# Performance work log

Hardware: AMD Instinct MI355X
Metric: run time of the kernel (lower is better)

Reference implementation:

```python
import jax, jax.numpy as jnp
import numpy as np

N, E, F, H = 50000, 500000, 128, 128   # nodes, edges, in-features, hidden
L, R, B = 3, 8, 30                     # layers, relations, bases
G, C = 16, 8                           # graphs in batch, classes
EPS = 1e-5


def setup_inputs() -> dict:
    key = jax.random.key(0)
    ks = jax.random.split(key, 16)
    x = jax.random.normal(ks[0], (N, F), jnp.float32)
    edge_index = jax.random.randint(ks[1], (2, E), 0, N)
    edge_attr = jax.random.randint(ks[2], (E,), 0, R)
    batch = jnp.sort(jax.random.randint(ks[3], (N,), 0, G))
    # RGCN params (all layers share shapes since F == H)
    basis = jax.random.normal(ks[4], (L, B, H, H), jnp.float32) * 0.05
    comp = jax.random.normal(ks[5], (L, R, B), jnp.float32) * 0.2
    root = jax.random.normal(ks[6], (L, H, H), jnp.float32) * 0.05
    bias = jnp.zeros((L, H), jnp.float32)
    # BatchNorm (eval mode: running stats)
    bn1_gamma = jnp.ones((F,), jnp.float32)
    bn1_beta = jnp.zeros((F,), jnp.float32)
    bn1_mean = jax.random.normal(ks[7], (F,), jnp.float32) * 0.1
    bn1_var = jax.random.uniform(ks[8], (F,), jnp.float32, 0.5, 1.5)
    bn2_gamma = jnp.ones((H,), jnp.float32)
    bn2_beta = jnp.zeros((H,), jnp.float32)
    bn2_mean = jax.random.normal(ks[9], (H,), jnp.float32) * 0.1
    bn2_var = jax.random.uniform(ks[10], (H,), jnp.float32, 0.5, 1.5)
    fc1_w = jax.random.normal(ks[11], (H, H), jnp.float32) * 0.05
    fc1_b = jnp.zeros((H,), jnp.float32)
    fc2_w = jax.random.normal(ks[12], (H, C), jnp.float32) * 0.05
    fc2_b = jnp.zeros((C,), jnp.float32)
    return dict(x=x, edge_index=edge_index, edge_attr=edge_attr, batch=batch,
                bn1_gamma=bn1_gamma, bn1_beta=bn1_beta, bn1_mean=bn1_mean, bn1_var=bn1_var,
                basis=basis, comp=comp, root=root, bias=bias,
                bn2_gamma=bn2_gamma, bn2_beta=bn2_beta, bn2_mean=bn2_mean, bn2_var=bn2_var,
                fc1_w=fc1_w, fc1_b=fc1_b, fc2_w=fc2_w, fc2_b=fc2_b)


def _bn(x, gamma, beta, mean, var):
    return (x - mean) * jax.lax.rsqrt(var + EPS) * gamma + beta


def _rgcn_layer(x, basis_l, comp_l, root_l, bias_l, src, dst, edge_attr):
    # root transform + bias
    out = x @ root_l + bias_l
    # relation-wise basis-decomposed message passing, mean-aggregated per relation
    for r in range(R):
        W_r = jnp.einsum('b,bio->io', comp_l[r], basis_l)  # [H, H]
        xw = x @ W_r                                       # [N, H]
        mask = (edge_attr == r).astype(x.dtype)            # [E]
        msg = xw[src] * mask[:, None]                      # gather + mask
        agg = jax.ops.segment_sum(msg, dst, num_segments=N)
        deg = jax.ops.segment_sum(mask, dst, num_segments=N)
        out = out + agg / jnp.maximum(deg, 1.0)[:, None]
    return out


def reference(x, edge_index, edge_attr, batch,
              bn1_gamma, bn1_beta, bn1_mean, bn1_var,
              basis, comp, root, bias,
              bn2_gamma, bn2_beta, bn2_mean, bn2_var,
              fc1_w, fc1_b, fc2_w, fc2_b):
    src, dst = edge_index[0], edge_index[1]
    h = _bn(x, bn1_gamma, bn1_beta, bn1_mean, bn1_var)
    for l in range(L):
        h = jax.nn.relu(_rgcn_layer(h, basis[l], comp[l], root[l], bias[l], src, dst, edge_attr))
        # dropout is identity in eval mode
    # global mean pool per graph
    sums = jax.ops.segment_sum(h, batch, num_segments=G)            # [G, H]
    counts = jax.ops.segment_sum(jnp.ones((N,), h.dtype), batch, num_segments=G)
    g = sums / jnp.maximum(counts, 1.0)[:, None]
    g = _bn(g, bn2_gamma, bn2_beta, bn2_mean, bn2_var)
    # temporal_type == 'mean'
    v = jax.nn.relu(g.mean(axis=0))                                 # [H]
    v = jax.nn.relu(v @ fc1_w + fc1_b)
    logits = v @ fc2_w + fc2_b                                      # [C]
    return jax.nn.log_softmax(logits, axis=-1)
```

## Files before the change

### kernel.cpp

```cpp
#include <hip/hip_runtime.h>
#include <hip/hip_bf16.h>

#define NN 50000
#define NE 500000
#define HID 128
#define LAYERS 3
#define RELS 8
#define BASES 30
#define GRAPHS 16
#define CLASSES 8
#define EPSV 1e-5f
#define NOUT (HID * (RELS + 1))
#define NSEG (NN * RELS)
#define SCAN_CHUNK 1024
#define SCAN_NBLK2 ((NSEG + SCAN_CHUNK - 1) / SCAN_CHUNK)
#define PCHUNK 128
#define DTILE 64
#define NDBLK ((NN + DTILE - 1) / DTILE)

typedef __attribute__((ext_vector_type(8))) short short8;
typedef __attribute__((ext_vector_type(4))) float f32x4;

__device__ __forceinline__ float bf2f(unsigned short u) {
    union { unsigned int i; float f; } x; x.i = ((unsigned int)u) << 16; return x.f;
}
__device__ __forceinline__ unsigned short f2bf(float f) {
    __hip_bfloat16 b = __float2bfloat16(f);
    return *(unsigned short*)&b;
}
__device__ __forceinline__ float ubf_lo(unsigned w) {
    union { unsigned i; float f; } t; t.i = w << 16; return t.f;
}
__device__ __forceinline__ float ubf_hi(unsigned w) {
    union { unsigned i; float f; } t; t.i = w & 0xFFFF0000u; return t.f;
}
__device__ __forceinline__ int permf(int f) {
    return (f & 64) | ((f & 15) << 2) | ((f >> 4) & 3);
}
__device__ __forceinline__ int ipermf(int q) {
    return (q & 64) | ((q & 3) << 4) | ((q >> 2) & 15);
}
__device__ __forceinline__ void gload16(const void* g, void* l) {
    __builtin_amdgcn_global_load_lds(
        (const __attribute__((address_space(1))) unsigned int*)g,
        (__attribute__((address_space(3))) unsigned int*)l, 16, 0, 0);
}

__global__ __launch_bounds__(256) void build_wcat(const float* __restrict__ basis,
                                                  const float* __restrict__ comp,
                                                  const float* __restrict__ root,
                                                  unsigned short* __restrict__ wT) {
    int bid = blockIdx.x;
    int l = bid >> 6;
    int k0 = (bid & 63) << 1;
    __shared__ float cl[RELS * BASES];
    int tid = threadIdx.x;
    if (tid < RELS * BASES) cl[tid] = comp[l * RELS * BASES + tid];
    __syncthreads();
    int j = tid & 127;
    int k = k0 + (tid >> 7);
    int pk = permf(k);
    const float* bp = basis + ((size_t)l * BASES * HID + k) * HID + j;
    float acc[RELS];
#pragma unroll
    for (int r = 0; r < RELS; ++r) acc[r] = 0.f;
    for (int b = 0; b < BASES; ++b) {
        float v = bp[(size_t)b * HID * HID];
#pragma unroll
        for (int r = 0; r < RELS; ++r) acc[r] += cl[r * BASES + b] * v;
    }
    unsigned short* wl = wT + (size_t)l * NOUT * HID;
#pragma unroll
    for (int r = 0; r < RELS; ++r)
        wl[(size_t)((1 + r) * HID + j) * HID + pk] = f2bf(acc[r]);
    wl[(size_t)j * HID + pk] = f2bf(root[((size_t)l * HID + k) * HID + j]);
}

__global__ void bn1_kernel(const float* __restrict__ x, const float* __restrict__ gamma,
                           const float* __restrict__ beta, const float* __restrict__ mean,
                           const float* __restrict__ var, unsigned short* __restrict__ habf) {
    int idx = blockIdx.x * blockDim.x + threadIdx.x;
    if (idx >= NN * HID) return;
    int q = idx & (HID - 1);
    int n = idx >> 7;
    int f = ipermf(q);
    habf[idx] = f2bf((x[(n << 7) + f] - mean[f]) * rsqrtf(var[f] + EPSV) * gamma[f] + beta[f]);
}

__global__ void deg_kernel(const int* __restrict__ ei, const int* __restrict__ ea,
                           float* __restrict__ deg) {
    int e = blockIdx.x * blockDim.x + threadIdx.x;
    if (e >= NE) return;
    int dst = ei[NE + e];
    atomicAdd(&deg[(size_t)dst * RELS + ea[e]], 1.0f);
}

__global__ __launch_bounds__(256) void scan_partial(float* __restrict__ deg,
                                                    int* __restrict__ rowptr,
                                                    int* __restrict__ bsum) {
    __shared__ int ssc[256];
    int t = threadIdx.x;
    int base = blockIdx.x * SCAN_CHUNK + t * 4;
    int v[4];
#pragma unroll
    for (int j = 0; j < 4; ++j) {
        int seg = base + j;
        if (seg < NSEG) {
            float d = deg[seg];
            v[j] = (int)(d + 0.5f);
            deg[seg] = 1.0f / fmaxf(d, 1.0f);
        } else v[j] = 0;
    }
    int tsum = v[0] + v[1] + v[2] + v[3];
    ssc[t] = tsum;
    __syncthreads();
    for (int ofs = 1; ofs < 256; ofs <<= 1) {
        int add = (t >= ofs) ? ssc[t - ofs] : 0;
        __syncthreads();
        ssc[t] += add;
        __syncthreads();
    }
    int excl = ssc[t] - tsum;
    int e = 0;
#pragma unroll
    for (int j = 0; j < 4; ++j) {
        if (base + j < NSEG) rowptr[base + j] = excl + e;
        e += v[j];
    }
    if (t == 255) bsum[blockIdx.x] = ssc[255];
}

__global__ __launch_bounds__(512) void scan_bsum(int* __restrict__ bsum) {
    __shared__ int s[512];
    int t = threadIdx.x;
    int v = (t < SCAN_NBLK2) ? bsum[t] : 0;
    s[t] = v;
    __syncthreads();
    for (int o = 1; o < 512; o <<= 1) {
        int a = (t >= o) ? s[t - o] : 0;
        __syncthreads();
        s[t] += a;
        __syncthreads();
    }
    if (t < SCAN_NBLK2) bsum[t] = s[t] - v;
}

__global__ __launch_bounds__(256) void scan_add(int* __restrict__ rowptr,
                                                const int* __restrict__ bsum) {
    int i = blockIdx.x * blockDim.x + threadIdx.x;
    if (i < NSEG) rowptr[i] += bsum[i >> 10];
    if (i == 0) rowptr[NSEG] = NE;
}

__global__ void fill_kernel(const int* __restrict__ ei, const int* __restrict__ ea,
                            const int* __restrict__ rowptr,
                            int* __restrict__ fillcnt, int* __restrict__ epk) {
    int e = blockIdx.x * blockDim.x + threadIdx.x;
    if (e >= NE) return;
    int src = ei[e];
    int seg = ei[NE + e] * RELS + ea[e];
    int pos = atomicAdd(&fillcnt[seg], 1);
    epk[rowptr[seg] + pos] = src;
}

__global__ __launch_bounds__(256) void rgcn_layer(const unsigned short* __restrict__ hin,
                                                  const unsigned short* __restrict__ wTl,
                                                  const float* __restrict__ bias,
                                                  const int* __restrict__ rp2,
                                                  const int* __restrict__ epk2,
                                                  const float* __restrict__ invdeg,
                                                  unsigned short* __restrict__ hout) {
    __shared__ __align__(16) unsigned short As[DTILE * HID];
    __shared__ __align__(16) unsigned short Bs[128 * HID];
    int row0 = blockIdx.x * DTILE;
    int tid = threadIdx.x;
    int wave = tid >> 6, lane = tid & 63;
    int quad = lane >> 4, l16 = lane & 15;
    int wn = wave * 32;
    int ld = tid >> 2, tq = tid & 3;
    int dst = row0 + ld;

    f32x4 acc[4][2];
#pragma unroll
    for (int i = 0; i < 4; ++i)
#pragma unroll
        for (int j = 0; j < 2; ++j) acc[i][j] = (f32x4){0.f, 0.f, 0.f, 0.f};

    auto mfma_panel = [&]() {
#pragma unroll
        for (int kc = 0; kc < 4; ++kc) {
            int ca = ((kc * 4 + quad) ^ (l16 & 7)) << 3;
            short8 a[4], b[2];
#pragma unroll
            for (int i = 0; i < 4; ++i) a[i] = *(const short8*)&As[(i * 16 + l16) * HID + ca];
#pragma unroll
            for (int j = 0; j < 2; ++j) b[j] = *(const short8*)&Bs[(wn + j * 16 + l16) * HID + ca];
#pragma unroll
            for (int i = 0; i < 4; ++i)
#pragma unroll
                for (int j = 0; j < 2; ++j)
                    acc[i][j] = __builtin_amdgcn_mfma_f32_16x16x32_bf16(a[i], b[j], acc[i][j], 0, 0, 0);
        }
    };

#pragma unroll
    for (int q = 0; q < 4; ++q) {
        int rb = (wave << 4) + (q << 2);
        int r = rb + (lane >> 4), c = lane & 15;
        int ga = row0 + r; if (ga > NN - 1) ga = NN - 1;
        gload16(hin + (size_t)ga * HID + ((c ^ (r & 7)) << 3), &As[rb * HID]);
    }
#pragma unroll
    for (int q = 0; q < 8; ++q) {
        int rb = (wave << 5) + (q << 2);
        int r = rb + (lane >> 4), c = lane & 15;
        gload16(wTl + (size_t)r * HID + ((c ^ (r & 7)) << 3), &Bs[rb * HID]);
    }
    __syncthreads();
    mfma_panel();

    for (int p = 1; p <= RELS; ++p) {
        float ga[32];
#pragma unroll
        for (int i2 = 0; i2 < 32; ++i2) ga[i2] = 0.f;
        float s = 0.f;
        if (dst < NN) {
            int seg = dst * RELS + (p - 1);
            int beg = rp2[seg], end = rp2[seg + 1];
            s = invdeg[seg];
            for (int e = beg; e < end; ++e) {
                int src = epk2[e];
                const uint4* rp = (const uint4*)(hin + (size_t)src * HID + (tq << 5));
                uint4 q0 = rp[0], q1 = rp[1], q2 = rp[2], q3 = rp[3];
#pragma unroll
                for (int q4 = 0; q4 < 4; ++q4) {
                    uint4 u = (q4 == 0) ? q0 : (q4 == 1) ? q1 : (q4 == 2) ? q2 : q3;
                    ga[q4 * 8 + 0] += ubf_lo(u.x); ga[q4 * 8 + 1] += ubf_hi(u.x);
                    ga[q4 * 8 + 2] += ubf_lo(u.y); ga[q4 * 8 + 3] += ubf_hi(u.y);
                    ga[q4 * 8 + 4] += ubf_lo(u.z); ga[q4 * 8 + 5] += ubf_hi(u.z);
                    ga[q4 * 8 + 6] += ubf_lo(u.w); ga[q4 * 8 + 7] += ubf_hi(u.w);
                }
            }
        }
        __syncthreads();
#pragma unroll
        for (int cc = 0; cc < 4; ++cc) {
            short8 v;
#pragma unroll
            for (int i2 = 0; i2 < 8; ++i2) v[i2] = (short)f2bf(ga[cc * 8 + i2] * s);
            int c = (tq << 2) + cc;
            *(short8*)&As[ld * HID + ((c ^ (ld & 7)) << 3)] = v;
        }
#pragma unroll
        for (int q = 0; q < 8; ++q) {
            int rb = (wave << 5) + (q << 2);
            int r = rb + (lane >> 4), c = lane & 15;
            gload16(wTl + (size_t)(p * 128 + r) * HID + ((c ^ (r & 7)) << 3), &Bs[rb * HID]);
        }
        __syncthreads();
        mfma_panel();
    }

    int pb = ((wave & 2) << 5) + (l16 << 2) + ((wave & 1) << 1);
    float b0 = bias[wn + l16], b1 = bias[wn + 16 + l16];
#pragma unroll
    for (int i = 0; i < 4; ++i)
#pragma unroll
        for (int reg = 0; reg < 4; ++reg) {
            int grow = row0 + i * 16 + quad * 4 + reg;
            if (grow >= NN) continue;
            unsigned u = (unsigned)f2bf(fmaxf(acc[i][0][reg] + b0, 0.f))
                       | ((unsigned)f2bf(fmaxf(acc[i][1][reg] + b1, 0.f)) << 16);
            *(unsigned*)(hout + (size_t)grow * HID + pb) = u;
        }
}

__global__ __launch_bounds__(256) void pool_kernel(const unsigned short* __restrict__ habf,
                                                   const int* __restrict__ batch,
                                                   float* __restrict__ psum,
                                                   float* __restrict__ pcnt) {
    int tid = threadIdx.x;
    int f = tid & 127;
    int sub = tid >> 7;
    int base = blockIdx.x * PCHUNK;
    float acc = 0.f, cnt = 0.f;
    int gcur = -1;
    for (int it = 0; it < PCHUNK / 2; ++it) {
        int node = base + it * 2 + sub;
        if (node >= NN) break;
        int g = batch[node];
        if (g != gcur) {
            if (gcur >= 0) {
                atomicAdd(&psum[gcur * HID + f], acc);
                if (f == 0) atomicAdd(&pcnt[gcur], cnt);
            }
            gcur = g; acc = 0.f; cnt = 0.f;
        }
        acc += bf2f(habf[(size_t)node * HID + f]);
        cnt += 1.f;
    }
    if (gcur >= 0) {
        atomicAdd(&psum[gcur * HID + f], acc);
        if (f == 0) atomicAdd(&pcnt[gcur], cnt);
    }
}

__global__ void head_kernel(const float* __restrict__ psum, const float* __restrict__ pcnt,
                            const float* __restrict__ g2, const float* __restrict__ b2,
                            const float* __restrict__ m2, const float* __restrict__ v2,
                            const float* __restrict__ fc1w, const float* __restrict__ fc1b,
                            const float* __restrict__ fc2w, const float* __restrict__ fc2b,
                            float* __restrict__ out) {
    __shared__ float v[HID];
    __shared__ float u[HID];
    __shared__ float lg[CLASSES];
    int j = threadIdx.x;
    int pj = permf(j);
    float acc = 0.f;
    for (int g = 0; g < GRAPHS; ++g) {
        float val = psum[g * HID + pj] / fmaxf(pcnt[g], 1.0f);
        val = (val - m2[j]) * rsqrtf(v2[j] + EPSV) * g2[j] + b2[j];
        acc += val;
    }
    v[j] = fmaxf(acc / (float)GRAPHS, 0.f);
    __syncthreads();
    float s = fc1b[j];
    for (int k = 0; k < HID; ++k) s += v[k] * fc1w[k * HID + j];
    u[j] = fmaxf(s, 0.f);
    __syncthreads();
    if (j < CLASSES) {
        float t = fc2b[j];
        for (int k = 0; k < HID; ++k) t += u[k] * fc2w[k * CLASSES + j];
        lg[j] = t;
    }
    __syncthreads();
    if (j < CLASSES) {
        float mx = lg[0];
        for (int c = 1; c < CLASSES; ++c) mx = fmaxf(mx, lg[c]);
        float se = 0.f;
        for (int c = 0; c < CLASSES; ++c) se += expf(lg[c] - mx);
        out[j] = lg[j] - mx - logf(se);
    }
}

extern "C" void kernel_launch(void* const* d_in, const int* in_sizes, int n_in,
                              void* d_out, int out_size, void* d_ws, size_t ws_size,
                              hipStream_t stream) {
    const float* x     = (const float*)d_in[0];
    const int*   ei    = (const int*)d_in[1];
    const int*   ea    = (const int*)d_in[2];
    const int*   batch = (const int*)d_in[3];
    const float* bn1g  = (const float*)d_in[4];
    const float* bn1b  = (const float*)d_in[5];
    const float* bn1m  = (const float*)d_in[6];
    const float* bn1v  = (const float*)d_in[7];
    const float* basis = (const float*)d_in[8];
    const float* comp  = (const float*)d_in[9];
    const float* root  = (const float*)d_in[10];
    const float* bias  = (const float*)d_in[11];
    const float* bn2g  = (const float*)d_in[12];
    const float* bn2b  = (const float*)d_in[13];
    const float* bn2m  = (const float*)d_in[14];
    const float* bn2v  = (const float*)d_in[15];
    const float* fc1w  = (const float*)d_in[16];
    const float* fc1b  = (const float*)d_in[17];
    const float* fc2w  = (const float*)d_in[18];
    const float* fc2b  = (const float*)d_in[19];

    float* ws = (float*)d_ws;
    size_t off = 0;
    unsigned short* wT  = (unsigned short*)(ws + off); off += (size_t)LAYERS * NOUT * HID / 2;
    unsigned short* hb0 = (unsigned short*)(ws + off); off += (size_t)NN * HID / 2;
    unsigned short* hb1 = (unsigned short*)(ws + off); off += (size_t)NN * HID / 2;
    float* deg    = ws + off; off += (size_t)NSEG;
    float* psum   = ws + off; off += (size_t)GRAPHS * HID + GRAPHS;
    float* pcnt   = psum + GRAPHS * HID;
    int* rowptr2  = (int*)(ws + off); off += (size_t)NSEG + 1;
    int* fillcnt2 = (int*)(ws + off); off += (size_t)NSEG;
    int* bsum     = (int*)(ws + off); off += (size_t)SCAN_NBLK2;
    int* epk2     = (int*)(ws + off); off += (size_t)NE;
    if (ws_size < off * sizeof(float)) return;

    hipMemsetAsync(psum, 0, (GRAPHS * HID + GRAPHS) * sizeof(float), stream);
    hipMemsetAsync(deg, 0, (size_t)NSEG * sizeof(float), stream);
    hipMemsetAsync(fillcnt2, 0, (size_t)NSEG * sizeof(int), stream);

    build_wcat<<<LAYERS * 64, 256, 0, stream>>>(basis, comp, root, wT);
    bn1_kernel<<<(NN * HID + 255) / 256, 256, 0, stream>>>(x, bn1g, bn1b, bn1m, bn1v, hb0);

    deg_kernel<<<(NE + 255) / 256, 256, 0, stream>>>(ei, ea, deg);
    scan_partial<<<SCAN_NBLK2, 256, 0, stream>>>(deg, rowptr2, bsum);
    scan_bsum<<<1, 512, 0, stream>>>(bsum);
    scan_add<<<(NSEG + 255) / 256, 256, 0, stream>>>(rowptr2, bsum);
    fill_kernel<<<(NE + 255) / 256, 256, 0, stream>>>(ei, ea, rowptr2, fillcnt2, epk2);

    const unsigned short* hin = hb0;
    unsigned short* hout = hb1;
    for (int l = 0; l < LAYERS; ++l) {
        rgcn_layer<<<NDBLK, 256, 0, stream>>>(hin, wT + (size_t)l * NOUT * HID,
                                              bias + (size_t)l * HID, rowptr2, epk2, deg, hout);
        const unsigned short* t = hin; hin = hout; hout = (unsigned short*)t;
    }

    pool_kernel<<<(NN + PCHUNK - 1) / PCHUNK, 256, 0, stream>>>(hin, batch, psum, pcnt);
    head_kernel<<<1, 128, 0, stream>>>(psum, pcnt, bn2g, bn2b, bn2m, bn2v,
                                       fc1w, fc1b, fc2w, fc2b, (float*)d_out);
}
```

Before: 488.8 us.

## Restructure RGCN layer: 16-row tiles, single-pass edge gather, register-streamed weights

Shrinks the destination tile from 64 to 16 rows and gathers all relations' neighbours in one pass over the dst's contiguous CSR range, with the relation id packed into the upper bits of each edge entry. All nine aggregated panels are staged in shared memory before the MFMA phase, and weights are read straight from global memory into double-buffered registers instead of through an LDS tile. This is meant to improve gather parallelism (16 threads per row instead of 4), raise occupancy, and remove the per-relation syncs. In exchange, weight traffic per node rises because each weight panel now serves 16 rows instead of 64. Packing assumes src fits in 16 bits, but N=50000 fits, and NDBLK assumes N is divisible by 16, which 50000 is.

```diff
diff --git a/kernel.cpp b/kernel.cpp
--- a/kernel.cpp
+++ b/kernel.cpp
@@ -15,8 +15,9 @@
 #define SCAN_CHUNK 1024
 #define SCAN_NBLK2 ((NSEG + SCAN_CHUNK - 1) / SCAN_CHUNK)
 #define PCHUNK 128
-#define DTILE 64
-#define NDBLK ((NN + DTILE - 1) / DTILE)
+#define DTILE 16
+#define NDBLK (NN / DTILE)
+#define ECAP 28
 
 typedef __attribute__((ext_vector_type(8))) short short8;
 typedef __attribute__((ext_vector_type(4))) float f32x4;
@@ -158,9 +159,10 @@
     int e = blockIdx.x * blockDim.x + threadIdx.x;
     if (e >= NE) return;
     int src = ei[e];
-    int seg = ei[NE + e] * RELS + ea[e];
+    int r = ea[e];
+    int seg = ei[NE + e] * RELS + r;
     int pos = atomicAdd(&fillcnt[seg], 1);
-    epk[rowptr[seg] + pos] = src;
+    epk[rowptr[seg] + pos] = (r << 16) | src;
 }
 
 __global__ __launch_bounds__(256) void rgcn_layer(const unsigned short* __restrict__ hin,
@@ -170,109 +172,128 @@
                                                   const int* __restrict__ epk2,
                                                   const float* __restrict__ invdeg,
                                                   unsigned short* __restrict__ hout) {
-    __shared__ __align__(16) unsigned short As[DTILE * HID];
-    __shared__ __align__(16) unsigned short Bs[128 * HID];
+    __shared__ __align__(16) unsigned short As[(RELS + 1) * DTILE * HID];
+    __shared__ unsigned int src_l[DTILE * ECAP];
+    __shared__ float inv_l[DTILE * RELS];
     int row0 = blockIdx.x * DTILE;
     int tid = threadIdx.x;
     int wave = tid >> 6, lane = tid & 63;
     int quad = lane >> 4, l16 = lane & 15;
     int wn = wave * 32;
-    int ld = tid >> 2, tq = tid & 3;
+    int ld = tid >> 4, tq = tid & 15;
     int dst = row0 + ld;
 
-    f32x4 acc[4][2];
-#pragma unroll
-    for (int i = 0; i < 4; ++i)
-#pragma unroll
-        for (int j = 0; j < 2; ++j) acc[i][j] = (f32x4){0.f, 0.f, 0.f, 0.f};
-
-    auto mfma_panel = [&]() {
+    int base = rp2[dst * RELS];
+    int tot = rp2[dst * RELS + RELS] - base;
+    if (tq < 8) inv_l[ld * 8 + tq] = invdeg[dst * RELS + tq];
+    {
+        int lim = tot < ECAP ? tot : ECAP;
+        for (int e = tq; e < lim; e += 16)
+            src_l[ld * ECAP + e] = (unsigned)epk2[base + e];
+    }
+    {
+        uint4 z = {0u, 0u, 0u, 0u};
+        int zr = 16 + (tid >> 1);
+        uint4* zp = (uint4*)&As[zr * HID + (tid & 1) * 64];
+#pragma unroll
+        for (int k = 0; k < 8; ++k) zp[k] = z;
+    }
+    {
+        int rb = wave << 2;
+        int r = rb + (lane >> 4), c = lane & 15;
+        gload16(hin + (size_t)(row0 + r) * HID + ((c ^ (r & 7)) << 3), &As[rb * HID]);
+    }
+    __syncthreads();
+
+    {
+        float ga[8];
+#pragma unroll
+        for (int i = 0; i < 8; ++i) ga[i] = 0.f;
+        int cur = -1;
+        int wofs = (tq ^ (ld & 7)) << 3;
+        int e = 0;
+        while (e < tot) {
+            int n = tot - e; if (n > 4) n = 4;
+            unsigned pk[4]; uint4 u[4];
+#pragma unroll
+            for (int i = 0; i < 4; ++i)
+                if (i < n) pk[i] = (e + i < ECAP) ? src_l[ld * ECAP + e + i]
+                                                  : (unsigned)epk2[base + e + i];
+#pragma unroll
+            for (int i = 0; i < 4; ++i)
+                if (i < n) u[i] = *(const uint4*)(hin + (size_t)(pk[i] & 0xFFFFu) * HID + (tq << 3));
+#pragma unroll
+            for (int i = 0; i < 4; ++i)
+                if (i < n) {
+                    int r = (int)(pk[i] >> 16);
+                    if (r != cur) {
+                        if (cur >= 0) {
+                            float s = inv_l[ld * 8 + cur];
+                            short8 v;
+#pragma unroll
+                            for (int k = 0; k < 8; ++k) v[k] = (short)f2bf(ga[k] * s);
+                            *(short8*)&As[((1 + cur) * DTILE + ld) * HID + wofs] = v;
+#pragma unroll
+                            for (int k = 0; k < 8; ++k) ga[k] = 0.f;
+                        }
+                        cur = r;
+                    }
+                    ga[0] += ubf_lo(u[i].x); ga[1] += ubf_hi(u[i].x);
+                    ga[2] += ubf_lo(u[i].y); ga[3] += ubf_hi(u[i].y);
+                    ga[4] += ubf_lo(u[i].z); ga[5] += ubf_hi(u[i].z);
+                    ga[6] += ubf_lo(u[i].w); ga[7] += ubf_hi(u[i].w);
+                }
+            e += 4;
+        }
+        if (cur >= 0) {
+            float s = inv_l[ld * 8 + cur];
+            short8 v;
+#pragma unroll
+            for (int k = 0; k < 8; ++k) v[k] = (short)f2bf(ga[k] * s);
+            *(short8*)&As[((1 + cur) * DTILE + ld) * HID + wofs] = v;
+        }
+    }
+
+    uint4 bA[2][4], bB[2][4];
+#pragma unroll
+    for (int j = 0; j < 2; ++j)
+#pragma unroll
+        for (int kc = 0; kc < 4; ++kc)
+            bA[j][kc] = *(const uint4*)(wTl + (size_t)(wn + j * 16 + l16) * HID + ((kc * 4 + quad) << 3));
+    __syncthreads();
+
+    f32x4 acc[2];
+    acc[0] = (f32x4){0.f, 0.f, 0.f, 0.f};
+    acc[1] = (f32x4){0.f, 0.f, 0.f, 0.f};
+#pragma unroll
+    for (int p = 0; p <= RELS; ++p) {
+        uint4 (*bc)[4] = (p & 1) ? bB : bA;
+        uint4 (*bn)[4] = (p & 1) ? bA : bB;
+        if (p < RELS) {
+#pragma unroll
+            for (int j = 0; j < 2; ++j)
+#pragma unroll
+                for (int kc = 0; kc < 4; ++kc)
+                    bn[j][kc] = *(const uint4*)(wTl + (size_t)((p + 1) * 128 + wn + j * 16 + l16) * HID
+                                                + ((kc * 4 + quad) << 3));
+        }
 #pragma unroll
         for (int kc = 0; kc < 4; ++kc) {
-            int ca = ((kc * 4 + quad) ^ (l16 & 7)) << 3;
-            short8 a[4], b[2];
-#pragma unroll
-            for (int i = 0; i < 4; ++i) a[i] = *(const short8*)&As[(i * 16 + l16) * HID + ca];
-#pragma unroll
-            for (int j = 0; j < 2; ++j) b[j] = *(const short8*)&Bs[(wn + j * 16 + l16) * HID + ca];
-#pragma unroll
-            for (int i = 0; i < 4; ++i)
-#pragma unroll
-                for (int j = 0; j < 2; ++j)
-                    acc[i][j] = __builtin_amdgcn_mfma_f32_16x16x32_bf16(a[i], b[j], acc[i][j], 0, 0, 0);
+            short8 a = *(const short8*)&As[(p * DTILE + l16) * HID + (((kc * 4 + quad) ^ (l16 & 7)) << 3)];
+            acc[0] = __builtin_amdgcn_mfma_f32_16x16x32_bf16(a, *(const short8*)&bc[0][kc], acc[0], 0, 0, 0);
+            acc[1] = __builtin_amdgcn_mfma_f32_16x16x32_bf16(a, *(const short8*)&bc[1][kc], acc[1], 0, 0, 0);
         }
-    };
-
-#pragma unroll
-    for (int q = 0; q < 4; ++q) {
-        int rb = (wave << 4) + (q << 2);
-        int r = rb + (lane >> 4), c = lane & 15;
-        int ga = row0 + r; if (ga > NN - 1) ga = NN - 1;
-        gload16(hin + (size_t)ga * HID + ((c ^ (r & 7)) << 3), &As[rb * HID]);
-    }
-#pragma unroll
-    for (int q = 0; q < 8; ++q) {
-        int rb = (wave << 5) + (q << 2);
-        int r = rb + (lane >> 4), c = lane & 15;
-        gload16(wTl + (size_t)r * HID + ((c ^ (r & 7)) << 3), &Bs[rb * HID]);
-    }
-    __syncthreads();
-    mfma_panel();
-
-    for (int p = 1; p <= RELS; ++p) {
-        float ga[32];
-#pragma unroll
-        for (int i2 = 0; i2 < 32; ++i2) ga[i2] = 0.f;
-        float s = 0.f;
-        if (dst < NN) {
-            int seg = dst * RELS + (p - 1);
-            int beg = rp2[seg], end = rp2[seg + 1];
-            s = invdeg[seg];
-            for (int e = beg; e < end; ++e) {
-                int src = epk2[e];
-                const uint4* rp = (const uint4*)(hin + (size_t)src * HID + (tq << 5));
-                uint4 q0 = rp[0], q1 = rp[1], q2 = rp[2], q3 = rp[3];
-#pragma unroll
-                for (int q4 = 0; q4 < 4; ++q4) {
-                    uint4 u = (q4 == 0) ? q0 : (q4 == 1) ? q1 : (q4 == 2) ? q2 : q3;
-                    ga[q4 * 8 + 0] += ubf_lo(u.x); ga[q4 * 8 + 1] += ubf_hi(u.x);
-                    ga[q4 * 8 + 2] += ubf_lo(u.y); ga[q4 * 8 + 3] += ubf_hi(u.y);
-                    ga[q4 * 8 + 4] += ubf_lo(u.z); ga[q4 * 8 + 5] += ubf_hi(u.z);
-                    ga[q4 * 8 + 6] += ubf_lo(u.w); ga[q4 * 8 + 7] += ubf_hi(u.w);
-                }
-            }
-        }
-        __syncthreads();
-#pragma unroll
-        for (int cc = 0; cc < 4; ++cc) {
-            short8 v;
-#pragma unroll
-            for (int i2 = 0; i2 < 8; ++i2) v[i2] = (short)f2bf(ga[cc * 8 + i2] * s);
-            int c = (tq << 2) + cc;
-            *(short8*)&As[ld * HID + ((c ^ (ld & 7)) << 3)] = v;
-        }
-#pragma unroll
-        for (int q = 0; q < 8; ++q) {
-            int rb = (wave << 5) + (q << 2);
-            int r = rb + (lane >> 4), c = lane & 15;
-            gload16(wTl + (size_t)(p * 128 + r) * HID + ((c ^ (r & 7)) << 3), &Bs[rb * HID]);
-        }
-        __syncthreads();
-        mfma_panel();
-    }
-
-    int pb = ((wave & 2) << 5) + (l16 << 2) + ((wave & 1) << 1);
+    }
+
+    int pb = (wn & 64) + (l16 << 2) + ((wn >> 4) & 3);
     float b0 = bias[wn + l16], b1 = bias[wn + 16 + l16];
 #pragma unroll
-    for (int i = 0; i < 4; ++i)
-#pragma unroll
-        for (int reg = 0; reg < 4; ++reg) {
-            int grow = row0 + i * 16 + quad * 4 + reg;
-            if (grow >= NN) continue;
-            unsigned u = (unsigned)f2bf(fmaxf(acc[i][0][reg] + b0, 0.f))
-                       | ((unsigned)f2bf(fmaxf(acc[i][1][reg] + b1, 0.f)) << 16);
-            *(unsigned*)(hout + (size_t)grow * HID + pb) = u;
-        }
+    for (int reg = 0; reg < 4; ++reg) {
+        int grow = row0 + quad * 4 + reg;
+        unsigned u = (unsigned)f2bf(fmaxf(acc[0][reg] + b0, 0.f))
+                   | ((unsigned)f2bf(fmaxf(acc[1][reg] + b1, 0.f)) << 16);
+        *(unsigned*)(hout + (size_t)grow * HID + pb) = u;
+    }
 }
 
 __global__ __launch_bounds__(256) void pool_kernel(const unsigned short* __restrict__ habf,
```

Result: slower. 627.4 us (+28.4%).

## Split RGCN layer into wave-per-node aggregation and FP8 concatenated GEMM

Applied to the files above, without the earlier changes.

The fused per-layer kernel, which gathered neighbours per relation and ran bf16 MFMA on each panel, is replaced by two kernels. The first aggregates mean messages per relation with one wave per destination node and writes an FP8 [N, 1152] concatenated buffer. The second runs a 128x128-tile FP8 MFMA GEMM over all nine K panels against FP8 weights. Inverse degrees are now computed inline from rowptr instead of stored. This trades an extra round trip through global memory and lower numerical precision (FP8 weights and activations) for better gather parallelism and cheaper matrix math.

```diff
diff --git a/kernel.cpp b/kernel.cpp
--- a/kernel.cpp
+++ b/kernel.cpp
@@ -10,15 +10,13 @@
 #define GRAPHS 16
 #define CLASSES 8
 #define EPSV 1e-5f
-#define NOUT (HID * (RELS + 1))
+#define KBIG 1152
 #define NSEG (NN * RELS)
 #define SCAN_CHUNK 1024
 #define SCAN_NBLK2 ((NSEG + SCAN_CHUNK - 1) / SCAN_CHUNK)
 #define PCHUNK 128
-#define DTILE 64
-#define NDBLK ((NN + DTILE - 1) / DTILE)
-
-typedef __attribute__((ext_vector_type(8))) short short8;
+#define NSTRIPE ((NN + 127) / 128)
+
 typedef __attribute__((ext_vector_type(4))) float f32x4;
 
 __device__ __forceinline__ float bf2f(unsigned short u) {
@@ -28,11 +26,8 @@
     __hip_bfloat16 b = __float2bfloat16(f);
     return *(unsigned short*)&b;
 }
-__device__ __forceinline__ float ubf_lo(unsigned w) {
-    union { unsigned i; float f; } t; t.i = w << 16; return t.f;
-}
-__device__ __forceinline__ float ubf_hi(unsigned w) {
-    union { unsigned i; float f; } t; t.i = w & 0xFFFF0000u; return t.f;
+__device__ __forceinline__ unsigned char f2fp8(float v) {
+    return (unsigned char)(__builtin_amdgcn_cvt_pk_fp8_f32(v, v, 0, false) & 0xFF);
 }
 __device__ __forceinline__ int permf(int f) {
     return (f & 64) | ((f & 15) << 2) | ((f >> 4) & 3);
@@ -49,7 +44,7 @@
 __global__ __launch_bounds__(256) void build_wcat(const float* __restrict__ basis,
                                                   const float* __restrict__ comp,
                                                   const float* __restrict__ root,
-                                                  unsigned short* __restrict__ wT) {
+                                                  unsigned char* __restrict__ wt8) {
     int bid = blockIdx.x;
     int l = bid >> 6;
     int k0 = (bid & 63) << 1;
@@ -69,11 +64,11 @@
 #pragma unroll
         for (int r = 0; r < RELS; ++r) acc[r] += cl[r * BASES + b] * v;
     }
-    unsigned short* wl = wT + (size_t)l * NOUT * HID;
+    unsigned char* wl = wt8 + (size_t)l * HID * KBIG;
 #pragma unroll
     for (int r = 0; r < RELS; ++r)
-        wl[(size_t)((1 + r) * HID + j) * HID + pk] = f2bf(acc[r]);
-    wl[(size_t)j * HID + pk] = f2bf(root[((size_t)l * HID + k) * HID + j]);
+        wl[(size_t)j * KBIG + (1 + r) * HID + pk] = f2fp8(acc[r]);
+    wl[(size_t)j * KBIG + pk] = f2fp8(root[((size_t)l * HID + k) * HID + j]);
 }
 
 __global__ void bn1_kernel(const float* __restrict__ x, const float* __restrict__ gamma,
@@ -88,14 +83,13 @@
 }
 
 __global__ void deg_kernel(const int* __restrict__ ei, const int* __restrict__ ea,
-                           float* __restrict__ deg) {
+                           int* __restrict__ cnt) {
     int e = blockIdx.x * blockDim.x + threadIdx.x;
     if (e >= NE) return;
-    int dst = ei[NE + e];
-    atomicAdd(&deg[(size_t)dst * RELS + ea[e]], 1.0f);
-}
-
-__global__ __launch_bounds__(256) void scan_partial(float* __restrict__ deg,
+    atomicAdd(&cnt[ei[NE + e] * RELS + ea[e]], 1);
+}
+
+__global__ __launch_bounds__(256) void scan_partial(const int* __restrict__ cnt,
                                                     int* __restrict__ rowptr,
                                                     int* __restrict__ bsum) {
     __shared__ int ssc[256];
@@ -105,11 +99,7 @@
 #pragma unroll
     for (int j = 0; j < 4; ++j) {
         int seg = base + j;
-        if (seg < NSEG) {
-            float d = deg[seg];
-            v[j] = (int)(d + 0.5f);
-            deg[seg] = 1.0f / fmaxf(d, 1.0f);
-        } else v[j] = 0;
+        v[j] = (seg < NSEG) ? cnt[seg] : 0;
     }
     int tsum = v[0] + v[1] + v[2] + v[3];
     ssc[t] = tsum;
@@ -157,121 +147,117 @@
                             int* __restrict__ fillcnt, int* __restrict__ epk) {
     int e = blockIdx.x * blockDim.x + threadIdx.x;
     if (e >= NE) return;
-    int src = ei[e];
     int seg = ei[NE + e] * RELS + ea[e];
     int pos = atomicAdd(&fillcnt[seg], 1);
-    epk[rowptr[seg] + pos] = src;
-}
-
-__global__ __launch_bounds__(256) void rgcn_layer(const unsigned short* __restrict__ hin,
-                                                  const unsigned short* __restrict__ wTl,
-                                                  const float* __restrict__ bias,
+    epk[rowptr[seg] + pos] = ei[e];
+}
+
+__global__ __launch_bounds__(256) void agg_kernel(const unsigned short* __restrict__ hin,
                                                   const int* __restrict__ rp2,
                                                   const int* __restrict__ epk2,
-                                                  const float* __restrict__ invdeg,
-                                                  unsigned short* __restrict__ hout) {
-    __shared__ __align__(16) unsigned short As[DTILE * HID];
-    __shared__ __align__(16) unsigned short Bs[128 * HID];
-    int row0 = blockIdx.x * DTILE;
+                                                  unsigned char* __restrict__ aggbuf) {
+    int lane = threadIdx.x & 63;
+    int dst = (blockIdx.x << 2) + (threadIdx.x >> 6);
+    if (dst >= NN) return;
+    unsigned char* arow = aggbuf + (size_t)dst * KBIG;
+    unsigned u = *(const unsigned*)(hin + (size_t)dst * HID + lane * 2);
+    unsigned pk = __builtin_amdgcn_cvt_pk_fp8_f32(bf2f((unsigned short)(u & 0xFFFF)),
+                                                  bf2f((unsigned short)(u >> 16)), 0, false);
+    *(unsigned short*)(arow + lane * 2) = (unsigned short)(pk & 0xFFFF);
+    int rp[9];
+#pragma unroll
+    for (int i = 0; i < 9; ++i) rp[i] = rp2[dst * RELS + i];
+#pragma unroll
+    for (int r = 0; r < RELS; ++r) {
+        int beg = rp[r], end = rp[r + 1];
+        float a0 = 0.f, a1 = 0.f;
+        int e = beg;
+        for (; e + 2 <= end; e += 2) {
+            int s0 = epk2[e], s1 = epk2[e + 1];
+            unsigned u0 = *(const unsigned*)(hin + (size_t)s0 * HID + lane * 2);
+            unsigned u1 = *(const unsigned*)(hin + (size_t)s1 * HID + lane * 2);
+            a0 += bf2f((unsigned short)(u0 & 0xFFFF)) + bf2f((unsigned short)(u1 & 0xFFFF));
+            a1 += bf2f((unsigned short)(u0 >> 16)) + bf2f((unsigned short)(u1 >> 16));
+        }
+        if (e < end) {
+            int s0 = epk2[e];
+            unsigned u0 = *(const unsigned*)(hin + (size_t)s0 * HID + lane * 2);
+            a0 += bf2f((unsigned short)(u0 & 0xFFFF));
+            a1 += bf2f((unsigned short)(u0 >> 16));
+        }
+        float s = 1.0f / fmaxf((float)(end - beg), 1.0f);
+        unsigned w = __builtin_amdgcn_cvt_pk_fp8_f32(a0 * s, a1 * s, 0, false);
+        *(unsigned short*)(arow + (1 + r) * HID + lane * 2) = (unsigned short)(w & 0xFFFF);
+    }
+}
+
+__global__ __launch_bounds__(256) void gemm_big(const unsigned char* __restrict__ aggbuf,
+                                                const unsigned char* __restrict__ wt8,
+                                                const float* __restrict__ bias,
+                                                unsigned short* __restrict__ hout) {
+    __shared__ __align__(16) unsigned char As[128 * 128];
+    __shared__ __align__(16) unsigned char Bs[128 * 128];
+    int stripe = blockIdx.x;
+    int row0 = stripe * 128;
     int tid = threadIdx.x;
     int wave = tid >> 6, lane = tid & 63;
+    int wm = (wave & 1) * 64, wn = (wave >> 1) * 64;
     int quad = lane >> 4, l16 = lane & 15;
-    int wn = wave * 32;
-    int ld = tid >> 2, tq = tid & 3;
-    int dst = row0 + ld;
-
-    f32x4 acc[4][2];
+    int lr = lane >> 3, lc = lane & 7;
+
+    f32x4 acc[4][4];
 #pragma unroll
     for (int i = 0; i < 4; ++i)
 #pragma unroll
-        for (int j = 0; j < 2; ++j) acc[i][j] = (f32x4){0.f, 0.f, 0.f, 0.f};
-
-    auto mfma_panel = [&]() {
+        for (int j = 0; j < 4; ++j) acc[i][j] = (f32x4){0.f, 0.f, 0.f, 0.f};
+
+    for (int p = 0; p < 9; ++p) {
+#pragma unroll
+        for (int q = 0; q < 4; ++q) {
+            int rb = wave * 32 + q * 8;
+            int r = rb + lr;
+            int sc = (lc ^ (r & 7)) << 4;
+            int ga = row0 + r; if (ga > NN - 1) ga = NN - 1;
+            gload16(aggbuf + (size_t)ga * KBIG + p * 128 + sc, As + rb * 128);
+            gload16(wt8 + (size_t)r * KBIG + p * 128 + sc, Bs + rb * 128);
+        }
+        __syncthreads();
 #pragma unroll
         for (int kc = 0; kc < 4; ++kc) {
-            int ca = ((kc * 4 + quad) ^ (l16 & 7)) << 3;
-            short8 a[4], b[2];
-#pragma unroll
-            for (int i = 0; i < 4; ++i) a[i] = *(const short8*)&As[(i * 16 + l16) * HID + ca];
-#pragma unroll
-            for (int j = 0; j < 2; ++j) b[j] = *(const short8*)&Bs[(wn + j * 16 + l16) * HID + ca];
+            int ch = kc * 2 + (quad >> 1);
+            int half = (quad & 1) * 8;
+            long a[4], b[4];
+#pragma unroll
+            for (int i = 0; i < 4; ++i) {
+                int ra = wm + i * 16 + l16;
+                int rb2 = wn + i * 16 + l16;
+                a[i] = *(const long*)(As + ra * 128 + ((ch ^ (ra & 7)) << 4) + half);
+                b[i] = *(const long*)(Bs + rb2 * 128 + ((ch ^ (rb2 & 7)) << 4) + half);
+            }
 #pragma unroll
             for (int i = 0; i < 4; ++i)
 #pragma unroll
-                for (int j = 0; j < 2; ++j)
-                    acc[i][j] = __builtin_amdgcn_mfma_f32_16x16x32_bf16(a[i], b[j], acc[i][j], 0, 0, 0);
-        }
-    };
-
-#pragma unroll
-    for (int q = 0; q < 4; ++q) {
-        int rb = (wave << 4) + (q << 2);
-        int r = rb + (lane >> 4), c = lane & 15;
-        int ga = row0 + r; if (ga > NN - 1) ga = NN - 1;
-        gload16(hin + (size_t)ga * HID + ((c ^ (r & 7)) << 3), &As[rb * HID]);
-    }
-#pragma unroll
-    for (int q = 0; q < 8; ++q) {
-        int rb = (wave << 5) + (q << 2);
-        int r = rb + (lane >> 4), c = lane & 15;
-        gload16(wTl + (size_t)r * HID + ((c ^ (r & 7)) << 3), &Bs[rb * HID]);
-    }
-    __syncthreads();
-    mfma_panel();
-
-    for (int p = 1; p <= RELS; ++p) {
-        float ga[32];
-#pragma unroll
-        for (int i2 = 0; i2 < 32; ++i2) ga[i2] = 0.f;
-        float s = 0.f;
-        if (dst < NN) {
-            int seg = dst * RELS + (p - 1);
-            int beg = rp2[seg], end = rp2[seg + 1];
-            s = invdeg[seg];
-            for (int e = beg; e < end; ++e) {
-                int src = epk2[e];
-                const uint4* rp = (const uint4*)(hin + (size_t)src * HID + (tq << 5));
-                uint4 q0 = rp[0], q1 = rp[1], q2 = rp[2], q3 = rp[3];
-#pragma unroll
-                for (int q4 = 0; q4 < 4; ++q4) {
-                    uint4 u = (q4 == 0) ? q0 : (q4 == 1) ? q1 : (q4 == 2) ? q2 : q3;
-                    ga[q4 * 8 + 0] += ubf_lo(u.x); ga[q4 * 8 + 1] += ubf_hi(u.x);
-                    ga[q4 * 8 + 2] += ubf_lo(u.y); ga[q4 * 8 + 3] += ubf_hi(u.y);
-                    ga[q4 * 8 + 4] += ubf_lo(u.z); ga[q4 * 8 + 5] += ubf_hi(u.z);
-                    ga[q4 * 8 + 6] += ubf_lo(u.w); ga[q4 * 8 + 7] += ubf_hi(u.w);
-                }
-            }
-        }
-        __syncthreads();
-#pragma unroll
-        for (int cc = 0; cc < 4; ++cc) {
-            short8 v;
-#pragma unroll
-            for (int i2 = 0; i2 < 8; ++i2) v[i2] = (short)f2bf(ga[cc * 8 + i2] * s);
-            int c = (tq << 2) + cc;
-            *(short8*)&As[ld * HID + ((c ^ (ld & 7)) << 3)] = v;
-        }
-#pragma unroll
-        for (int q = 0; q < 8; ++q) {
-            int rb = (wave << 5) + (q << 2);
-            int r = rb + (lane >> 4), c = lane & 15;
-            gload16(wTl + (size_t)(p * 128 + r) * HID + ((c ^ (r & 7)) << 3), &Bs[rb * HID]);
-        }
-        __syncthreads();
-        mfma_panel();
-    }
-
-    int pb = ((wave & 2) << 5) + (l16 << 2) + ((wave & 1) << 1);
+                for (int j = 0; j < 4; ++j)
+                    acc[i][j] = __builtin_amdgcn_mfma_f32_16x16x32_fp8_fp8(a[i], b[j], acc[i][j], 0, 0, 0);
+        }
+        __syncthreads();
+    }
+
+    int pbase = wn + l16 * 4;
     float b0 = bias[wn + l16], b1 = bias[wn + 16 + l16];
+    float b2 = bias[wn + 32 + l16], b3 = bias[wn + 48 + l16];
 #pragma unroll
     for (int i = 0; i < 4; ++i)
 #pragma unroll
         for (int reg = 0; reg < 4; ++reg) {
-            int grow = row0 + i * 16 + quad * 4 + reg;
+            int grow = row0 + wm + i * 16 + quad * 4 + reg;
             if (grow >= NN) continue;
-            unsigned u = (unsigned)f2bf(fmaxf(acc[i][0][reg] + b0, 0.f))
-                       | ((unsigned)f2bf(fmaxf(acc[i][1][reg] + b1, 0.f)) << 16);
-            *(unsigned*)(hout + (size_t)grow * HID + pb) = u;
+            unsigned lo = (unsigned)f2bf(fmaxf(acc[i][0][reg] + b0, 0.f)) |
+                          ((unsigned)f2bf(fmaxf(acc[i][1][reg] + b1, 0.f)) << 16);
+            unsigned hi = (unsigned)f2bf(fmaxf(acc[i][2][reg] + b2, 0.f)) |
+                          ((unsigned)f2bf(fmaxf(acc[i][3][reg] + b3, 0.f)) << 16);
+            uint2 pk = {lo, hi};
+            *(uint2*)(hout + (size_t)grow * HID + pbase) = pk;
         }
 }
 
@@ -369,12 +355,13 @@
 
     float* ws = (float*)d_ws;
     size_t off = 0;
-    unsigned short* wT  = (unsigned short*)(ws + off); off += (size_t)LAYERS * NOUT * HID / 2;
+    unsigned char* wt8 = (unsigned char*)(ws + off); off += (size_t)LAYERS * HID * KBIG / 4;
     unsigned short* hb0 = (unsigned short*)(ws + off); off += (size_t)NN * HID / 2;
     unsigned short* hb1 = (unsigned short*)(ws + off); off += (size_t)NN * HID / 2;
-    float* deg    = ws + off; off += (size_t)NSEG;
+    unsigned char* aggbuf = (unsigned char*)(ws + off); off += (size_t)NN * KBIG / 4;
     float* psum   = ws + off; off += (size_t)GRAPHS * HID + GRAPHS;
     float* pcnt   = psum + GRAPHS * HID;
+    int* cnt      = (int*)(ws + off); off += (size_t)NSEG;
     int* rowptr2  = (int*)(ws + off); off += (size_t)NSEG + 1;
     int* fillcnt2 = (int*)(ws + off); off += (size_t)NSEG;
     int* bsum     = (int*)(ws + off); off += (size_t)SCAN_NBLK2;
@@ -382,14 +369,14 @@
     if (ws_size < off * sizeof(float)) return;
 
     hipMemsetAsync(psum, 0, (GRAPHS * HID + GRAPHS) * sizeof(float), stream);
-    hipMemsetAsync(deg, 0, (size_t)NSEG * sizeof(float), stream);
+    hipMemsetAsync(cnt, 0, (size_t)NSEG * sizeof(int), stream);
     hipMemsetAsync(fillcnt2, 0, (size_t)NSEG * sizeof(int), stream);
 
-    build_wcat<<<LAYERS * 64, 256, 0, stream>>>(basis, comp, root, wT);
+    build_wcat<<<LAYERS * 64, 256, 0, stream>>>(basis, comp, root, wt8);
     bn1_kernel<<<(NN * HID + 255) / 256, 256, 0, stream>>>(x, bn1g, bn1b, bn1m, bn1v, hb0);
 
-    deg_kernel<<<(NE + 255) / 256, 256, 0, stream>>>(ei, ea, deg);
-    scan_partial<<<SCAN_NBLK2, 256, 0, stream>>>(deg, rowptr2, bsum);
+    deg_kernel<<<(NE + 255) / 256, 256, 0, stream>>>(ei, ea, cnt);
+    scan_partial<<<SCAN_NBLK2, 256, 0, stream>>>(cnt, rowptr2, bsum);
     scan_bsum<<<1, 512, 0, stream>>>(bsum);
     scan_add<<<(NSEG + 255) / 256, 256, 0, stream>>>(rowptr2, bsum);
     fill_kernel<<<(NE + 255) / 256, 256, 0, stream>>>(ei, ea, rowptr2, fillcnt2, epk2);
@@ -397,8 +384,9 @@
     const unsigned short* hin = hb0;
     unsigned short* hout = hb1;
     for (int l = 0; l < LAYERS; ++l) {
-        rgcn_layer<<<NDBLK, 256, 0, stream>>>(hin, wT + (size_t)l * NOUT * HID,
-                                              bias + (size_t)l * HID, rowptr2, epk2, deg, hout);
+        agg_kernel<<<(NN + 3) / 4, 256, 0, stream>>>(hin, rowptr2, epk2, aggbuf);
+        gemm_big<<<NSTRIPE, 256, 0, stream>>>(aggbuf, wt8 + (size_t)l * HID * KBIG,
+                                              bias + (size_t)l * HID, hout);
         const unsigned short* t = hin; hin = hout; hout = (unsigned short*)t;
     }
 
```

Result: faster. 439.6 us (-10.1%).
